# Kernel optimization log

Hardware: AMD Instinct MI355X
Metric: run time of the kernel (lower is better)

The kernel has to match this reference:

```python
import jax, jax.numpy as jnp
import numpy as np

HIDDEN = 1024
HEADS = 16
HEAD_DIM = HIDDEN // HEADS  # 64


def setup_inputs() -> dict:
    key = jax.random.key(0)
    ks = jax.random.split(key, 5)
    B, S = 1, 4096
    inputs = jax.random.normal(ks[0], (B, S, HIDDEN), dtype=jnp.float32)
    # Xavier-uniform-ish init for square [out, in] weights (torch Linear layout)
    lim = float(np.sqrt(6.0 / (HIDDEN + HIDDEN)))
    def w(k):
        return jax.random.uniform(k, (HIDDEN, HIDDEN), jnp.float32, -lim, lim)
    return {
        "inputs": inputs,
        "Wq": w(ks[1]), "bq": jnp.zeros((HIDDEN,), jnp.float32),
        "Wk": w(ks[2]), "bk": jnp.zeros((HIDDEN,), jnp.float32),
        "Wv": w(ks[3]), "bv": jnp.zeros((HIDDEN,), jnp.float32),
        "Wo": w(ks[4]), "bo": jnp.zeros((HIDDEN,), jnp.float32),
    }


def reference(inputs, Wq, bq, Wk, bk, Wv, bv, Wo, bo):
    # Chunked online-softmax attention (causal_mask=False) is mathematically
    # identical to standard softmax multi-head attention.
    B, S, _ = inputs.shape
    def proj(W, b):
        # torch Linear: x @ W.T + b, then split heads -> [B, S, H, D]
        return (inputs @ W.T + b).reshape(B, S, HEADS, HEAD_DIM)
    q = proj(Wq, bq) / jnp.asarray(np.sqrt(HEAD_DIM), inputs.dtype)
    k = proj(Wk, bk)
    v = proj(Wv, bv)
    scores = jnp.einsum("bqhd,bkhd->bhqk", q, k)          # [B, H, S, S]
    attn = jax.nn.softmax(scores, axis=-1)
    ctx = jnp.einsum("bhqk,bkhd->bqhd", attn, v)           # [B, S, H, D]
    ctx = ctx.reshape(B, S, HIDDEN)
    return ctx @ Wo.T + bo
```

## Files before the change

kernel.cpp:

```cpp
#include <hip/hip_runtime.h>
#include <hip/hip_bf16.h>

typedef float f32x4 __attribute__((ext_vector_type(4)));
typedef float f32x16 __attribute__((ext_vector_type(16)));
typedef unsigned short u16x8 __attribute__((ext_vector_type(8)));
typedef unsigned int u32x2 __attribute__((ext_vector_type(2)));
typedef unsigned int u32x4 __attribute__((ext_vector_type(4)));
typedef __bf16 b16x8 __attribute__((ext_vector_type(8)));

static __device__ __forceinline__ unsigned short f2bf(float f) {
    unsigned int u = __builtin_bit_cast(unsigned int, f);
    return (unsigned short)((u + 0x7fffu + ((u >> 16) & 1u)) >> 16);
}

static __device__ __forceinline__ unsigned int pkbf(float a, float b) {
    unsigned short x = __builtin_bit_cast(unsigned short, (__bf16)a);
    unsigned short y = __builtin_bit_cast(unsigned short, (__bf16)b);
    return (unsigned int)x | ((unsigned int)y << 16);
}

static __device__ __forceinline__ f32x4 mfma16(u16x8 a, u16x8 b, f32x4 c) {
    return __builtin_amdgcn_mfma_f32_16x16x32_bf16(
        __builtin_bit_cast(b16x8, a), __builtin_bit_cast(b16x8, b), c, 0, 0, 0);
}

static __device__ __forceinline__ f32x16 mfma32(u16x8 a, u16x8 b, f32x16 c) {
    return __builtin_amdgcn_mfma_f32_32x32x16_bf16(
        __builtin_bit_cast(b16x8, a), __builtin_bit_cast(b16x8, b), c, 0, 0, 0);
}

__global__ __launch_bounds__(256)
void convert_all(const float* __restrict__ x,
                 const float* __restrict__ wq, const float* __restrict__ wk,
                 const float* __restrict__ wv,
                 unsigned short* __restrict__ xb,
                 unsigned short* __restrict__ wqb, unsigned short* __restrict__ wkb,
                 unsigned short* __restrict__ wvb)
{
    const int bk = (int)blockIdx.x;
    const float* src;
    unsigned short* dst;
    int base;
    if (bk < 2048) { src = x; dst = xb; base = bk; }
    else {
        int wi = (bk - 2048) >> 9;
        src = (wi == 0) ? wq : (wi == 1) ? wk : wv;
        dst = (wi == 0) ? wqb : (wi == 1) ? wkb : wvb;
        base = (bk - 2048) & 511;
    }
    size_t i = ((size_t)base * 256 + threadIdx.x) * 8;
    f32x4 a = *reinterpret_cast<const f32x4*>(&src[i]);
    f32x4 b = *reinterpret_cast<const f32x4*>(&src[i + 4]);
    u16x8 r;
    r[0] = f2bf(a[0]); r[1] = f2bf(a[1]); r[2] = f2bf(a[2]); r[3] = f2bf(a[3]);
    r[4] = f2bf(b[0]); r[5] = f2bf(b[1]); r[6] = f2bf(b[2]); r[7] = f2bf(b[3]);
    *reinterpret_cast<u16x8*>(&dst[i]) = r;
}

template<bool OUT_F32, int MODE>
__global__ __launch_bounds__(256)
void gemm_k(const unsigned short* __restrict__ A,
            const unsigned short* __restrict__ B0, const unsigned short* __restrict__ B1,
            const unsigned short* __restrict__ B2,
            const float* __restrict__ bias0, const float* __restrict__ bias1,
            const float* __restrict__ bias2,
            void* c0, void* c1, void* c2,
            int K, float scale0)
{
    __shared__ unsigned short As[128][32];
    __shared__ unsigned short Bs[128][32];
    const int t = (int)threadIdx.x;
    const int wave = t >> 6, lane = t & 63;
    const int wr = wave >> 1, wc = wave & 1;
    const int lo = lane & 15, g = lane >> 4;

    const int bid = (int)blockIdx.x;
    int rowb, colb;
    if constexpr (MODE == 0) {
        const int x = bid & 7, c = bid >> 3;
        rowb = (x >> 1) * 8 + (c & 7);
        colb = (x & 1) * 12 + (c >> 3);
    } else {
        colb = bid & 7; rowb = bid >> 3;
    }
    const int brow = rowb * 128, bcol = colb * 128;
    const int w = bcol >> 10;
    const int segcol = bcol & 1023;
    const unsigned short* Bw = (w == 0) ? B0 : (w == 1) ? B1 : B2;
    const float* bi = (w == 0) ? bias0 : (w == 1) ? bias1 : bias2;
    const float scale = (w == 0) ? scale0 : 1.0f;

    const int row0 = t >> 2, c8 = t & 3;
    const int row1 = row0 + 64;

    f32x4 acc[4][4] = {};
    u16x8 aReg[2], bReg[2];

    aReg[0] = *reinterpret_cast<const u16x8*>(&A[(size_t)(brow + row0) * K + c8 * 8]);
    aReg[1] = *reinterpret_cast<const u16x8*>(&A[(size_t)(brow + row1) * K + c8 * 8]);
    bReg[0] = *reinterpret_cast<const u16x8*>(&Bw[(size_t)(segcol + row0) * K + c8 * 8]);
    bReg[1] = *reinterpret_cast<const u16x8*>(&Bw[(size_t)(segcol + row1) * K + c8 * 8]);

    for (int kt = 0; kt < K; kt += 32) {
        __syncthreads();
        *reinterpret_cast<u16x8*>(&As[row0][c8 * 8]) = aReg[0];
        *reinterpret_cast<u16x8*>(&As[row1][c8 * 8]) = aReg[1];
        *reinterpret_cast<u16x8*>(&Bs[row0][c8 * 8]) = bReg[0];
        *reinterpret_cast<u16x8*>(&Bs[row1][c8 * 8]) = bReg[1];
        __syncthreads();

        int ktn = kt + 32; if (ktn >= K) ktn = 0;
        aReg[0] = *reinterpret_cast<const u16x8*>(&A[(size_t)(brow + row0) * K + ktn + c8 * 8]);
        aReg[1] = *reinterpret_cast<const u16x8*>(&A[(size_t)(brow + row1) * K + ktn + c8 * 8]);
        bReg[0] = *reinterpret_cast<const u16x8*>(&Bw[(size_t)(segcol + row0) * K + ktn + c8 * 8]);
        bReg[1] = *reinterpret_cast<const u16x8*>(&Bw[(size_t)(segcol + row1) * K + ktn + c8 * 8]);

        u16x8 af[4], bf[4];
        #pragma unroll
        for (int mf = 0; mf < 4; ++mf)
            af[mf] = *reinterpret_cast<const u16x8*>(&As[wr * 64 + mf * 16 + lo][g * 8]);
        #pragma unroll
        for (int nf = 0; nf < 4; ++nf)
            bf[nf] = *reinterpret_cast<const u16x8*>(&Bs[wc * 64 + nf * 16 + lo][g * 8]);
        #pragma unroll
        for (int mf = 0; mf < 4; ++mf)
            #pragma unroll
            for (int nf = 0; nf < 4; ++nf)
                acc[mf][nf] = mfma16(af[mf], bf[nf], acc[mf][nf]);
    }

    void* cp = (w == 0) ? c0 : (w == 1) ? c1 : c2;
    #pragma unroll
    for (int nf = 0; nf < 4; ++nf) {
        int colLocal = wc * 64 + nf * 16 + lo;
        int cw = segcol + colLocal;
        float bv = bi[cw];
        if (MODE == 0 && w == 2) {
            #pragma unroll
            for (int mf = 0; mf < 4; ++mf) {
                int rowb2 = brow + wr * 64 + mf * 16 + g * 4;
                ushort4 u;
                u.x = f2bf(acc[mf][nf][0] + bv);
                u.y = f2bf(acc[mf][nf][1] + bv);
                u.z = f2bf(acc[mf][nf][2] + bv);
                u.w = f2bf(acc[mf][nf][3] + bv);
                *reinterpret_cast<ushort4*>(
                    &((unsigned short*)cp)[(size_t)cw * 4096 + rowb2]) = u;
            }
        } else {
            #pragma unroll
            for (int mf = 0; mf < 4; ++mf) {
                #pragma unroll
                for (int j = 0; j < 4; ++j) {
                    int row = brow + wr * 64 + mf * 16 + g * 4 + j;
                    float v = (acc[mf][nf][j] + bv) * scale;
                    if constexpr (OUT_F32)
                        ((float*)cp)[(size_t)row * 1024 + cw] = v;
                    else
                        ((unsigned short*)cp)[(size_t)row * 1024 + cw] = f2bf(v);
                }
            }
        }
    }
}

template<int SPLIT>
__global__ __launch_bounds__(256, 2 * SPLIT)
void attn_kernel(const unsigned short* __restrict__ Q,
                 const unsigned short* __restrict__ Kg,
                 const unsigned short* __restrict__ VTg,
                 unsigned short* __restrict__ Ctx,
                 float* __restrict__ Op, float* __restrict__ Lp)
{
    __shared__ unsigned short lds[2][2][4096];
    const int t = (int)threadIdx.x;
    const int lane = t & 63;
    const int q5 = lane & 31;
    const int hi = lane >> 5;
    const int bid = (int)blockIdx.x;
    const int sp = (SPLIT == 2) ? (bid >> 9) : 0;
    const int inner = bid & 511;
    const int h = (inner & 7) | (((inner >> 3) & 1) << 3);
    const int qb = inner >> 4;
    const int hc = h * 64;
    const int wv = t >> 6;
    const int qbase = qb * 128 + wv * 32;
    const int kt0 = sp * (4096 / SPLIT);
    const int NT = 4096 / (SPLIT * 64);

    const int sr = t >> 3, sch = t & 7;
    const int f0 = (sr ^ (sr >> 3)) & 7;
    const int scol0 = (sch ^ f0) * 8;
    const int scol1 = (sch ^ f0 ^ 4) * 8;
    const int sdst = sr * 64 + sch * 8;

    u16x8 qf[4];
    #pragma unroll
    for (int kf = 0; kf < 4; ++kf)
        qf[kf] = *reinterpret_cast<const u16x8*>(
            &Q[(size_t)(qbase + q5) * 1024 + hc + kf * 16 + hi * 8]);

    f32x16 o0 = {}, o1 = {};
    float lsum = 0.f;

    {
        u16x8 k0 = *reinterpret_cast<const u16x8*>(&Kg[(size_t)(kt0 + sr) * 1024 + hc + scol0]);
        u16x8 k1 = *reinterpret_cast<const u16x8*>(&Kg[(size_t)(kt0 + sr + 32) * 1024 + hc + scol1]);
        u16x8 v0 = *reinterpret_cast<const u16x8*>(&VTg[(size_t)(hc + sr) * 4096 + kt0 + scol0]);
        u16x8 v1 = *reinterpret_cast<const u16x8*>(&VTg[(size_t)(hc + sr + 32) * 4096 + kt0 + scol1]);
        *reinterpret_cast<u16x8*>(&lds[0][0][sdst]) = k0;
        *reinterpret_cast<u16x8*>(&lds[0][0][sdst + 2048]) = k1;
        *reinterpret_cast<u16x8*>(&lds[0][1][sdst]) = v0;
        *reinterpret_cast<u16x8*>(&lds[0][1][sdst + 2048]) = v1;
    }

    const int sz0 = (q5 ^ (q5 >> 3)) & 7;
    const int sz1 = sz0 ^ 4;
    int cur = 0;

    for (int tt = 0; tt < NT; ++tt) {
        __syncthreads();

        const int ktn = kt0 + (((tt + 1) & (NT - 1)) << 6);
        u16x8 kn0 = *reinterpret_cast<const u16x8*>(&Kg[(size_t)(ktn + sr) * 1024 + hc + scol0]);
        u16x8 kn1 = *reinterpret_cast<const u16x8*>(&Kg[(size_t)(ktn + sr + 32) * 1024 + hc + scol1]);
        u16x8 vn0 = *reinterpret_cast<const u16x8*>(&VTg[(size_t)(hc + sr) * 4096 + ktn + scol0]);
        u16x8 vn1 = *reinterpret_cast<const u16x8*>(&VTg[(size_t)(hc + sr + 32) * 4096 + ktn + scol1]);

        const unsigned short* Kb = lds[cur][0];
        const unsigned short* Vb = lds[cur][1];

        f32x16 s0 = {}, s1 = {};
        #pragma unroll
        for (int kf = 0; kf < 4; ++kf) {
            int off0 = ((kf * 2 + hi) ^ sz0) * 8;
            int off1 = ((kf * 2 + hi) ^ sz1) * 8;
            u16x8 ka0 = *reinterpret_cast<const u16x8*>(&Kb[q5 * 64 + off0]);
            u16x8 ka1 = *reinterpret_cast<const u16x8*>(&Kb[(q5 + 32) * 64 + off1]);
            s0 = mfma32(ka0, qf[kf], s0);
            s1 = mfma32(ka1, qf[kf], s1);
        }

        unsigned int u0[8], u1[8];
        float ps = 0.f;
        #pragma unroll
        for (int r = 0; r < 8; ++r) {
            float e0 = __builtin_amdgcn_exp2f(s0[2 * r]);
            float e1 = __builtin_amdgcn_exp2f(s0[2 * r + 1]);
            float e2 = __builtin_amdgcn_exp2f(s1[2 * r]);
            float e3 = __builtin_amdgcn_exp2f(s1[2 * r + 1]);
            ps += (e0 + e1) + (e2 + e3);
            u0[r] = pkbf(e0, e1);
            u1[r] = pkbf(e2, e3);
        }
        ps += __shfl_xor(ps, 32);
        lsum += ps;

        u16x8 pa[4];
        #pragma unroll
        for (int b = 0; b < 2; ++b) {
            #pragma unroll
            for (int ks = 0; ks < 2; ++ks) {
                unsigned int x0 = b ? u1[4 * ks]     : u0[4 * ks];
                unsigned int x1 = b ? u1[4 * ks + 1] : u0[4 * ks + 1];
                unsigned int y0 = b ? u1[4 * ks + 2] : u0[4 * ks + 2];
                unsigned int y1 = b ? u1[4 * ks + 3] : u0[4 * ks + 3];
                u32x2 r0 = __builtin_amdgcn_permlane32_swap(x0, y0, false, false);
                u32x2 r1 = __builtin_amdgcn_permlane32_swap(x1, y1, false, false);
                u32x4 d;
                d[0] = r0[0]; d[1] = r1[0]; d[2] = r0[1]; d[3] = r1[1];
                pa[2 * b + ks] = __builtin_bit_cast(u16x8, d);
            }
        }

        #pragma unroll
        for (int ks = 0; ks < 4; ++ks) {
            int off0 = ((ks * 2 + hi) ^ sz0) * 8;
            int off1 = ((ks * 2 + hi) ^ sz1) * 8;
            u16x8 vb0 = *reinterpret_cast<const u16x8*>(&Vb[q5 * 64 + off0]);
            u16x8 vb1 = *reinterpret_cast<const u16x8*>(&Vb[(q5 + 32) * 64 + off1]);
            o0 = mfma32(pa[ks], vb0, o0);
            o1 = mfma32(pa[ks], vb1, o1);
        }

        unsigned short* Kw = lds[cur ^ 1][0];
        unsigned short* Vw = lds[cur ^ 1][1];
        *reinterpret_cast<u16x8*>(&Kw[sdst]) = kn0;
        *reinterpret_cast<u16x8*>(&Kw[sdst + 2048]) = kn1;
        *reinterpret_cast<u16x8*>(&Vw[sdst]) = vn0;
        *reinterpret_cast<u16x8*>(&Vw[sdst + 2048]) = vn1;
        cur ^= 1;
    }

    if constexpr (SPLIT == 1) {
        float linv = 1.f / lsum;
        #pragma unroll
        for (int r = 0; r < 16; ++r) {
            int qr = (r & 3) + 8 * (r >> 2) + 4 * hi;
            float lr = __shfl(linv, qr);
            size_t row = (size_t)(qbase + qr) * 1024 + hc;
            Ctx[row + q5]      = f2bf(o0[r] * lr);
            Ctx[row + 32 + q5] = f2bf(o1[r] * lr);
        }
    } else {
        const int pb = (sp << 9) + (h * 32 + qb);
        float* op = Op + ((size_t)pb * 128 + wv * 32) * 64;
        #pragma unroll
        for (int r = 0; r < 16; ++r) {
            int qr = (r & 3) + 8 * (r >> 2) + 4 * hi;
            op[(size_t)qr * 64 + q5]      = o0[r];
            op[(size_t)qr * 64 + 32 + q5] = o1[r];
        }
        if (hi == 0)
            Lp[(size_t)pb * 128 + wv * 32 + q5] = lsum;
    }
}

__global__ __launch_bounds__(256)
void combine2(const float* __restrict__ Op, const float* __restrict__ Lp,
              unsigned short* __restrict__ Ctx,
              const float* __restrict__ Wo, unsigned short* __restrict__ wob)
{
    const int bk = (int)blockIdx.x;
    const int t = (int)threadIdx.x;
    if (bk >= 512) {
        size_t i = ((size_t)(bk - 512) * 256 + t) * 8;
        f32x4 a = *reinterpret_cast<const f32x4*>(&Wo[i]);
        f32x4 b = *reinterpret_cast<const f32x4*>(&Wo[i + 4]);
        u16x8 r;
        r[0] = f2bf(a[0]); r[1] = f2bf(a[1]); r[2] = f2bf(a[2]); r[3] = f2bf(a[3]);
        r[4] = f2bf(b[0]); r[5] = f2bf(b[1]); r[6] = f2bf(b[2]); r[7] = f2bf(b[3]);
        *reinterpret_cast<u16x8*>(&wob[i]) = r;
        return;
    }
    const int b = bk;
    const int h = b >> 5, qb = b & 31;
    const int r = t >> 1, dh = (t & 1) * 32;
    const size_t i0 = ((size_t)b * 128 + r) * 64 + dh;
    const size_t i1 = ((size_t)(512 + b) * 128 + r) * 64 + dh;
    const float l = Lp[(size_t)b * 128 + r] + Lp[(size_t)(512 + b) * 128 + r];
    const float inv = 1.f / l;
    const int row = qb * 128 + r;
    unsigned short* dst = &Ctx[(size_t)row * 1024 + h * 64 + dh];
    #pragma unroll
    for (int d = 0; d < 32; d += 8) {
        f32x4 a0 = *reinterpret_cast<const f32x4*>(&Op[i0 + d]);
        f32x4 a1 = *reinterpret_cast<const f32x4*>(&Op[i0 + d + 4]);
        f32x4 b0 = *reinterpret_cast<const f32x4*>(&Op[i1 + d]);
        f32x4 b1 = *reinterpret_cast<const f32x4*>(&Op[i1 + d + 4]);
        u16x8 o;
        #pragma unroll
        for (int j = 0; j < 4; ++j) {
            o[j]     = f2bf((a0[j] + b0[j]) * inv);
            o[4 + j] = f2bf((a1[j] + b1[j]) * inv);
        }
        *reinterpret_cast<u16x8*>(&dst[d]) = o;
    }
}

extern "C" void kernel_launch(void* const* d_in, const int* in_sizes, int n_in,
                              void* d_out, int out_size, void* d_ws, size_t ws_size,
                              hipStream_t stream)
{
    const float* x  = (const float*)d_in[0];
    const float* Wq = (const float*)d_in[1];
    const float* bq = (const float*)d_in[2];
    const float* Wk = (const float*)d_in[3];
    const float* bk = (const float*)d_in[4];
    const float* Wv = (const float*)d_in[5];
    const float* bv = (const float*)d_in[6];
    const float* Wo = (const float*)d_in[7];
    const float* bo = (const float*)d_in[8];
    float* out = (float*)d_out;

    const int S = 4096, HID = 1024;
    const size_t MB = 1u << 20;
    unsigned short* xb  = (unsigned short*)d_ws;
    unsigned short* qws = xb + (size_t)S * HID;
    unsigned short* kws = qws + (size_t)S * HID;
    unsigned short* vtw = kws + (size_t)S * HID;
    unsigned short* cws = xb;
    float* Op = (float*)((char*)d_ws + 32 * MB);
    float* Lp = (float*)((char*)d_ws + 64 * MB);
    unsigned short* wqb = (unsigned short*)((char*)d_ws + 32 * MB);
    unsigned short* wkb = wqb + (size_t)HID * HID;
    unsigned short* wvb = wkb + (size_t)HID * HID;
    unsigned short* wob = qws;

    const float qscale = 0.125f * 1.44269504088896f;

    convert_all<<<3584, 256, 0, stream>>>(x, Wq, Wk, Wv, xb, wqb, wkb, wvb);

    gemm_k<false, 0><<<768, 256, 0, stream>>>(xb, wqb, wkb, wvb, bq, bk, bv,
                                              qws, kws, vtw, HID, qscale);

    attn_kernel<2><<<1024, 256, 0, stream>>>(qws, kws, vtw, cws, Op, Lp);

    combine2<<<1024, 256, 0, stream>>>(Op, Lp, cws, Wo, wob);

    gemm_k<true, 1><<<256, 256, 0, stream>>>(cws, wob, wob, wob, bo, bo, bo,
                                             out, out, out, HID, 1.0f);
}
```

Measured before the change: 175.8 us.

## Use direct global-to-LDS loads in QKV GEMM and MFMA row sums in attention

The QKV projection GEMM now loads tiles with global_load_lds straight into shared memory instead of staging them through registers with a software prefetch. This drops the register round trip but also loses the overlap of the next tile's load with compute. In the attention kernel, the softmax row sum is now computed by an extra MFMA against a ones vector instead of scalar adds plus a cross-lane shuffle. That moves VALU work onto the matrix unit at the cost of one more MFMA per k-step and some extra accumulator registers. The output GEMM is split into its own kernel, keeping the old register-staged path.

```diff
diff --git a/kernel.cpp b/kernel.cpp
--- a/kernel.cpp
+++ b/kernel.cpp
@@ -27,6 +27,12 @@
 static __device__ __forceinline__ f32x16 mfma32(u16x8 a, u16x8 b, f32x16 c) {
     return __builtin_amdgcn_mfma_f32_32x32x16_bf16(
         __builtin_bit_cast(b16x8, a), __builtin_bit_cast(b16x8, b), c, 0, 0, 0);
+}
+
+static __device__ __forceinline__ void gload16(const void* g, void* l) {
+    __builtin_amdgcn_global_load_lds(
+        (const __attribute__((address_space(1))) void*)g,
+        (__attribute__((address_space(3))) void*)l, 16, 0, 0);
 }
 
 __global__ __launch_bounds__(256)
@@ -57,15 +63,14 @@
     *reinterpret_cast<u16x8*>(&dst[i]) = r;
 }
 
-template<bool OUT_F32, int MODE>
 __global__ __launch_bounds__(256)
-void gemm_k(const unsigned short* __restrict__ A,
-            const unsigned short* __restrict__ B0, const unsigned short* __restrict__ B1,
-            const unsigned short* __restrict__ B2,
-            const float* __restrict__ bias0, const float* __restrict__ bias1,
-            const float* __restrict__ bias2,
-            void* c0, void* c1, void* c2,
-            int K, float scale0)
+void gemm_qkv(const unsigned short* __restrict__ A,
+              const unsigned short* __restrict__ B0, const unsigned short* __restrict__ B1,
+              const unsigned short* __restrict__ B2,
+              const float* __restrict__ bias0, const float* __restrict__ bias1,
+              const float* __restrict__ bias2,
+              void* c0, void* c1, void* c2,
+              int K, float scale0)
 {
     __shared__ unsigned short As[128][32];
     __shared__ unsigned short Bs[128][32];
@@ -75,14 +80,9 @@
     const int lo = lane & 15, g = lane >> 4;
 
     const int bid = (int)blockIdx.x;
-    int rowb, colb;
-    if constexpr (MODE == 0) {
-        const int x = bid & 7, c = bid >> 3;
-        rowb = (x >> 1) * 8 + (c & 7);
-        colb = (x & 1) * 12 + (c >> 3);
-    } else {
-        colb = bid & 7; rowb = bid >> 3;
-    }
+    const int xc = bid & 7, c = bid >> 3;
+    const int rowb = (xc >> 1) * 8 + (c & 7);
+    const int colb = (xc & 1) * 12 + (c >> 3);
     const int brow = rowb * 128, bcol = colb * 128;
     const int w = bcol >> 10;
     const int segcol = bcol & 1023;
@@ -90,30 +90,19 @@
     const float* bi = (w == 0) ? bias0 : (w == 1) ? bias1 : bias2;
     const float scale = (w == 0) ? scale0 : 1.0f;
 
-    const int row0 = t >> 2, c8 = t & 3;
-    const int row1 = row0 + 64;
+    const int glr = lane >> 2, glc = (lane & 3) * 8;
 
     f32x4 acc[4][4] = {};
-    u16x8 aReg[2], bReg[2];
-
-    aReg[0] = *reinterpret_cast<const u16x8*>(&A[(size_t)(brow + row0) * K + c8 * 8]);
-    aReg[1] = *reinterpret_cast<const u16x8*>(&A[(size_t)(brow + row1) * K + c8 * 8]);
-    bReg[0] = *reinterpret_cast<const u16x8*>(&Bw[(size_t)(segcol + row0) * K + c8 * 8]);
-    bReg[1] = *reinterpret_cast<const u16x8*>(&Bw[(size_t)(segcol + row1) * K + c8 * 8]);
 
     for (int kt = 0; kt < K; kt += 32) {
         __syncthreads();
-        *reinterpret_cast<u16x8*>(&As[row0][c8 * 8]) = aReg[0];
-        *reinterpret_cast<u16x8*>(&As[row1][c8 * 8]) = aReg[1];
-        *reinterpret_cast<u16x8*>(&Bs[row0][c8 * 8]) = bReg[0];
-        *reinterpret_cast<u16x8*>(&Bs[row1][c8 * 8]) = bReg[1];
+        #pragma unroll
+        for (int i = 0; i < 2; ++i) {
+            int r = wave * 32 + i * 16;
+            gload16(&A[(size_t)(brow + r + glr) * K + kt + glc], &As[r][0]);
+            gload16(&Bw[(size_t)(segcol + r + glr) * K + kt + glc], &Bs[r][0]);
+        }
         __syncthreads();
-
-        int ktn = kt + 32; if (ktn >= K) ktn = 0;
-        aReg[0] = *reinterpret_cast<const u16x8*>(&A[(size_t)(brow + row0) * K + ktn + c8 * 8]);
-        aReg[1] = *reinterpret_cast<const u16x8*>(&A[(size_t)(brow + row1) * K + ktn + c8 * 8]);
-        bReg[0] = *reinterpret_cast<const u16x8*>(&Bw[(size_t)(segcol + row0) * K + ktn + c8 * 8]);
-        bReg[1] = *reinterpret_cast<const u16x8*>(&Bw[(size_t)(segcol + row1) * K + ktn + c8 * 8]);
 
         u16x8 af[4], bf[4];
         #pragma unroll
@@ -135,7 +124,7 @@
         int colLocal = wc * 64 + nf * 16 + lo;
         int cw = segcol + colLocal;
         float bv = bi[cw];
-        if (MODE == 0 && w == 2) {
+        if (w == 2) {
             #pragma unroll
             for (int mf = 0; mf < 4; ++mf) {
                 int rowb2 = brow + wr * 64 + mf * 16 + g * 4;
@@ -153,14 +142,77 @@
                 #pragma unroll
                 for (int j = 0; j < 4; ++j) {
                     int row = brow + wr * 64 + mf * 16 + g * 4 + j;
-                    float v = (acc[mf][nf][j] + bv) * scale;
-                    if constexpr (OUT_F32)
-                        ((float*)cp)[(size_t)row * 1024 + cw] = v;
-                    else
-                        ((unsigned short*)cp)[(size_t)row * 1024 + cw] = f2bf(v);
+                    ((unsigned short*)cp)[(size_t)row * 1024 + cw] =
+                        f2bf((acc[mf][nf][j] + bv) * scale);
                 }
             }
         }
+    }
+}
+
+__global__ __launch_bounds__(256)
+void gemm_o(const unsigned short* __restrict__ A, const unsigned short* __restrict__ Bw,
+            const float* __restrict__ bi, float* __restrict__ cp, int K)
+{
+    __shared__ unsigned short As[128][32];
+    __shared__ unsigned short Bs[128][32];
+    const int t = (int)threadIdx.x;
+    const int wave = t >> 6, lane = t & 63;
+    const int wr = wave >> 1, wc = wave & 1;
+    const int lo = lane & 15, g = lane >> 4;
+    const int bid = (int)blockIdx.x;
+    const int brow = (bid >> 3) * 128, bcol = (bid & 7) * 128;
+
+    const int row0 = t >> 2, c8 = t & 3;
+    const int row1 = row0 + 64;
+
+    f32x4 acc[4][4] = {};
+    u16x8 aReg[2], bReg[2];
+
+    aReg[0] = *reinterpret_cast<const u16x8*>(&A[(size_t)(brow + row0) * K + c8 * 8]);
+    aReg[1] = *reinterpret_cast<const u16x8*>(&A[(size_t)(brow + row1) * K + c8 * 8]);
+    bReg[0] = *reinterpret_cast<const u16x8*>(&Bw[(size_t)(bcol + row0) * K + c8 * 8]);
+    bReg[1] = *reinterpret_cast<const u16x8*>(&Bw[(size_t)(bcol + row1) * K + c8 * 8]);
+
+    for (int kt = 0; kt < K; kt += 32) {
+        __syncthreads();
+        *reinterpret_cast<u16x8*>(&As[row0][c8 * 8]) = aReg[0];
+        *reinterpret_cast<u16x8*>(&As[row1][c8 * 8]) = aReg[1];
+        *reinterpret_cast<u16x8*>(&Bs[row0][c8 * 8]) = bReg[0];
+        *reinterpret_cast<u16x8*>(&Bs[row1][c8 * 8]) = bReg[1];
+        __syncthreads();
+
+        int ktn = kt + 32; if (ktn >= K) ktn = 0;
+        aReg[0] = *reinterpret_cast<const u16x8*>(&A[(size_t)(brow + row0) * K + ktn + c8 * 8]);
+        aReg[1] = *reinterpret_cast<const u16x8*>(&A[(size_t)(brow + row1) * K + ktn + c8 * 8]);
+        bReg[0] = *reinterpret_cast<const u16x8*>(&Bw[(size_t)(bcol + row0) * K + ktn + c8 * 8]);
+        bReg[1] = *reinterpret_cast<const u16x8*>(&Bw[(size_t)(bcol + row1) * K + ktn + c8 * 8]);
+
+        u16x8 af[4], bf[4];
+        #pragma unroll
+        for (int mf = 0; mf < 4; ++mf)
+            af[mf] = *reinterpret_cast<const u16x8*>(&As[wr * 64 + mf * 16 + lo][g * 8]);
+        #pragma unroll
+        for (int nf = 0; nf < 4; ++nf)
+            bf[nf] = *reinterpret_cast<const u16x8*>(&Bs[wc * 64 + nf * 16 + lo][g * 8]);
+        #pragma unroll
+        for (int mf = 0; mf < 4; ++mf)
+            #pragma unroll
+            for (int nf = 0; nf < 4; ++nf)
+                acc[mf][nf] = mfma16(af[mf], bf[nf], acc[mf][nf]);
+    }
+
+    #pragma unroll
+    for (int nf = 0; nf < 4; ++nf) {
+        int cw = bcol + wc * 64 + nf * 16 + lo;
+        float bv = bi[cw];
+        #pragma unroll
+        for (int mf = 0; mf < 4; ++mf)
+            #pragma unroll
+            for (int j = 0; j < 4; ++j) {
+                int row = brow + wr * 64 + mf * 16 + g * 4 + j;
+                cp[(size_t)row * 1024 + cw] = acc[mf][nf][j] + bv;
+            }
     }
 }
 
@@ -200,8 +252,11 @@
         qf[kf] = *reinterpret_cast<const u16x8*>(
             &Q[(size_t)(qbase + q5) * 1024 + hc + kf * 16 + hi * 8]);
 
-    f32x16 o0 = {}, o1 = {};
-    float lsum = 0.f;
+    u16x8 vones;
+    #pragma unroll
+    for (int j = 0; j < 8; ++j) vones[j] = 0x3F80;
+
+    f32x16 o0 = {}, o1 = {}, lacc = {};
 
     {
         u16x8 k0 = *reinterpret_cast<const u16x8*>(&Kg[(size_t)(kt0 + sr) * 1024 + hc + scol0]);
@@ -242,19 +297,13 @@
         }
 
         unsigned int u0[8], u1[8];
-        float ps = 0.f;
         #pragma unroll
         for (int r = 0; r < 8; ++r) {
-            float e0 = __builtin_amdgcn_exp2f(s0[2 * r]);
-            float e1 = __builtin_amdgcn_exp2f(s0[2 * r + 1]);
-            float e2 = __builtin_amdgcn_exp2f(s1[2 * r]);
-            float e3 = __builtin_amdgcn_exp2f(s1[2 * r + 1]);
-            ps += (e0 + e1) + (e2 + e3);
-            u0[r] = pkbf(e0, e1);
-            u1[r] = pkbf(e2, e3);
-        }
-        ps += __shfl_xor(ps, 32);
-        lsum += ps;
+            u0[r] = pkbf(__builtin_amdgcn_exp2f(s0[2 * r]),
+                         __builtin_amdgcn_exp2f(s0[2 * r + 1]));
+            u1[r] = pkbf(__builtin_amdgcn_exp2f(s1[2 * r]),
+                         __builtin_amdgcn_exp2f(s1[2 * r + 1]));
+        }
 
         u16x8 pa[4];
         #pragma unroll
@@ -281,6 +330,7 @@
             u16x8 vb1 = *reinterpret_cast<const u16x8*>(&Vb[(q5 + 32) * 64 + off1]);
             o0 = mfma32(pa[ks], vb0, o0);
             o1 = mfma32(pa[ks], vb1, o1);
+            lacc = mfma32(pa[ks], vones, lacc);
         }
 
         unsigned short* Kw = lds[cur ^ 1][0];
@@ -293,11 +343,10 @@
     }
 
     if constexpr (SPLIT == 1) {
-        float linv = 1.f / lsum;
         #pragma unroll
         for (int r = 0; r < 16; ++r) {
             int qr = (r & 3) + 8 * (r >> 2) + 4 * hi;
-            float lr = __shfl(linv, qr);
+            float lr = 1.f / lacc[r];
             size_t row = (size_t)(qbase + qr) * 1024 + hc;
             Ctx[row + q5]      = f2bf(o0[r] * lr);
             Ctx[row + 32 + q5] = f2bf(o1[r] * lr);
@@ -311,8 +360,13 @@
             op[(size_t)qr * 64 + q5]      = o0[r];
             op[(size_t)qr * 64 + 32 + q5] = o1[r];
         }
-        if (hi == 0)
-            Lp[(size_t)pb * 128 + wv * 32 + q5] = lsum;
+        if (q5 == 0) {
+            #pragma unroll
+            for (int r = 0; r < 16; ++r) {
+                int qr = (r & 3) + 8 * (r >> 2) + 4 * hi;
+                Lp[(size_t)pb * 128 + wv * 32 + qr] = lacc[r];
+            }
+        }
     }
 }
 
@@ -391,13 +445,12 @@
 
     convert_all<<<3584, 256, 0, stream>>>(x, Wq, Wk, Wv, xb, wqb, wkb, wvb);
 
-    gemm_k<false, 0><<<768, 256, 0, stream>>>(xb, wqb, wkb, wvb, bq, bk, bv,
-                                              qws, kws, vtw, HID, qscale);
+    gemm_qkv<<<768, 256, 0, stream>>>(xb, wqb, wkb, wvb, bq, bk, bv,
+                                      qws, kws, vtw, HID, qscale);
 
     attn_kernel<2><<<1024, 256, 0, stream>>>(qws, kws, vtw, cws, Op, Lp);
 
     combine2<<<1024, 256, 0, stream>>>(Op, Lp, cws, Wo, wob);
 
-    gemm_k<true, 1><<<256, 256, 0, stream>>>(cws, wob, wob, wob, bo, bo, bo,
-                                             out, out, out, HID, 1.0f);
-}
+    gemm_o<<<256, 256, 0, stream>>>(cws, wob, bo, out, HID);
+}
```

Result: slower. 185.5 us (+5.5%).
